# Kernel tuning notes

Measured on AMD Instinct MI355X. Metric: run time of the kernel, lower is better.

Reference implementation:

```python
import jax, jax.numpy as jnp
import numpy as np

B, CDD, L, T, H, NH = 16, 10, 64, 128, 768, 12
DH = H // NH          # head dim = 64
S = CDD * L + T       # full sequence = 768 (640 candidate tokens + 128 terms)


def setup_inputs() -> dict:
    key = jax.random.key(0)
    ks = jax.random.split(key, 7)
    w = 0.02
    return {
        "hidden_states": jax.random.normal(ks[0], (B, S, H), jnp.float32),
        "Wq": jax.random.normal(ks[1], (H, H), jnp.float32) * w,
        "bq": jax.random.normal(ks[2], (H,), jnp.float32) * w,
        "Wk": jax.random.normal(ks[3], (H, H), jnp.float32) * w,
        "bk": jax.random.normal(ks[4], (H,), jnp.float32) * w,
        "Wv": jax.random.normal(ks[5], (H, H), jnp.float32) * w,
        "bv": jax.random.normal(ks[6], (H,), jnp.float32) * w,
    }


def _one_pass_mask(dtype):
    # block-diagonal over candidates + dense global columns for terms
    block = jnp.kron(jnp.eye(CDD, dtype=dtype), jnp.ones((L, L), dtype=dtype))  # [CDD*L, CDD*L]
    return jnp.concatenate([block, jnp.ones((CDD * L, T), dtype=dtype)], axis=-1)  # [CDD*L, S]


def reference(hidden_states, Wq, bq, Wk, bk, Wv, bv):
    def split_heads(x):  # [B, s, H] -> [B, NH, s, DH]
        return x.reshape(B, -1, NH, DH).transpose(0, 2, 1, 3)

    attn_field = hidden_states[:, :-T]                     # [B, CDD*L, H] queries only
    q = split_heads(attn_field @ Wq.T + bq)                # [B, NH, CDD*L, DH]
    k = split_heads(hidden_states @ Wk.T + bk)             # [B, NH, S, DH]
    v = split_heads(hidden_states @ Wv.T + bv)             # [B, NH, S, DH]

    mask = _one_pass_mask(q.dtype)                         # [CDD*L, S]
    scale = 1.0 / np.sqrt(DH).astype(np.float32)
    # NOTE: original multiplies scores by the mask (masked entries become 0, not -inf)
    scores = jnp.einsum('bhqd,bhkd->bhqk', q, k) * scale * mask
    probs = jax.nn.softmax(scores, axis=-1)                # [B, NH, CDD*L, S]

    ctx = jnp.einsum('bhqk,bhkd->bhqd', probs, v)          # [B, NH, CDD*L, DH]
    ctx = jnp.concatenate([ctx, v[:, :, -T:]], axis=2)     # append term values untouched
    return ctx.transpose(0, 2, 1, 3).reshape(B, S, H)
```

## Files before the change

kernel.cpp:

```cpp
#include <hip/hip_runtime.h>

constexpr int Bb  = 16;
constexpr int CDD = 10;
constexpr int Lc  = 64;
constexpr int T   = 128;
constexpr int H   = 768;
constexpr int NH  = 12;
constexpr int DH  = 64;
constexpr int S   = 768;
constexpr int SQ  = 640;
constexpr int MROWS = Bb * S;

typedef __attribute__((ext_vector_type(8))) short bf16x8;
typedef __attribute__((ext_vector_type(4))) short bf16x4;
typedef __attribute__((ext_vector_type(4))) float f32x4;

__device__ inline unsigned short f2bf(float f) {
  unsigned u = __float_as_uint(f);
  u += 0x7fff + ((u >> 16) & 1);
  return (unsigned short)(u >> 16);
}
__device__ inline float bf2f(unsigned short h) {
  return __uint_as_float(((unsigned)h) << 16);
}

__device__ inline void gld_lds16(const void* g, void* l) {
  __builtin_amdgcn_global_load_lds(
      (const __attribute__((address_space(1))) void*)g,
      (__attribute__((address_space(3))) void*)l, 16, 0, 0);
}

__device__ inline bf16x8 ld_b64x2(const unsigned short* p) {
  union { bf16x8 v; bf16x4 h[2]; } u;
  u.h[0] = *(const bf16x4*)p;
  u.h[1] = *(const bf16x4*)(p + 4);
  return u.v;
}

constexpr int NX4 = MROWS * H / 4;
constexpr int NW4 = H * H / 4;
__global__ void convert_all(const float* __restrict__ X,
                            const float* __restrict__ Wq,
                            const float* __restrict__ Wk,
                            const float* __restrict__ Wv,
                            unsigned short* __restrict__ Xb,
                            unsigned short* __restrict__ Wb) {
  int i = blockIdx.x * blockDim.x + threadIdx.x;
  const int stride = gridDim.x * blockDim.x;
  const int total = NX4 + 3 * NW4;
  for (; i < total; i += stride) {
    const float* src;
    unsigned short* dst;
    int off;
    if (i < NX4) {
      src = X; dst = Xb; off = i;
    } else {
      int k = i - NX4;
      int w = k / NW4;
      off = k - w * NW4;
      src = (w == 0) ? Wq : (w == 1) ? Wk : Wv;
      dst = Wb + (size_t)w * H * H;
    }
    float4 v = ((const float4*)src)[off];
    ushort4 o;
    o.x = f2bf(v.x); o.y = f2bf(v.y); o.z = f2bf(v.z); o.w = f2bf(v.w);
    ((ushort4*)dst)[off] = o;
  }
}

__launch_bounds__(256, 4)
__global__ void qkv_gemm(const unsigned short* __restrict__ Xb,
                         const unsigned short* __restrict__ Wb,
                         const float* __restrict__ bq, const float* __restrict__ bk,
                         const float* __restrict__ bv,
                         unsigned short* __restrict__ Qb, unsigned short* __restrict__ Kb,
                         unsigned short* __restrict__ Vb,
                         float* __restrict__ part,
                         float* __restrict__ out) {
  const int z = blockIdx.z;
  if (z == 0 && (blockIdx.x % 6) == 5) return;
  const unsigned short* W = Wb + (size_t)z * H * H;
  const float* bias = (z == 0) ? bq : (z == 1) ? bk : bv;
  unsigned short* Y = (z == 0) ? Qb : (z == 1) ? Kb : Vb;

  const int i0 = blockIdx.x * 128;
  const int j0 = blockIdx.y * 128;
  const int tid = threadIdx.x;
  const int wave = tid >> 6, lane = tid & 63;
  const int wr = wave >> 1, wc = wave & 1;
  const int col = lane & 15, quad = lane >> 4;

  __shared__ unsigned short As[128 * 32];
  __shared__ unsigned short Bs[128 * 32];

  f32x4 acc[4][4];
#pragma unroll
  for (int i = 0; i < 4; i++)
#pragma unroll
    for (int j = 0; j < 4; j++) acc[i][j] = (f32x4){0.f, 0.f, 0.f, 0.f};

  const int rowA0 = tid >> 2, csA0 = tid & 3;
  const int rowA1 = (tid + 256) >> 2, csA1 = tid & 3;
  const int gcA0 = csA0 ^ ((rowA0 >> 1) & 3);
  const int gcA1 = csA1 ^ ((rowA1 >> 1) & 3);

  for (int kt = 0; kt < 24; kt++) {
    const int k0 = kt * 32;
    gld_lds16(Xb + (size_t)(i0 + rowA0) * H + k0 + gcA0 * 8, &As[tid * 8]);
    gld_lds16(Xb + (size_t)(i0 + rowA1) * H + k0 + gcA1 * 8, &As[(tid + 256) * 8]);
    gld_lds16(W  + (size_t)(j0 + rowA0) * H + k0 + gcA0 * 8, &Bs[tid * 8]);
    gld_lds16(W  + (size_t)(j0 + rowA1) * H + k0 + gcA1 * 8, &Bs[(tid + 256) * 8]);
    __builtin_amdgcn_s_waitcnt(0);
    __syncthreads();

    bf16x8 a[4], b[4];
#pragma unroll
    for (int mt = 0; mt < 4; mt++) {
      int r = wr * 64 + mt * 16 + col;
      a[mt] = *(const bf16x8*)&As[r * 32 + ((quad ^ ((r >> 1) & 3)) * 8)];
    }
#pragma unroll
    for (int nt = 0; nt < 4; nt++) {
      int r = wc * 64 + nt * 16 + col;
      b[nt] = *(const bf16x8*)&Bs[r * 32 + ((quad ^ ((r >> 1) & 3)) * 8)];
    }
#pragma unroll
    for (int mt = 0; mt < 4; mt++)
#pragma unroll
      for (int nt = 0; nt < 4; nt++)
        acc[mt][nt] = __builtin_amdgcn_mfma_f32_16x16x32_bf16(a[mt], b[nt], acc[mt][nt], 0, 0, 0);
    __syncthreads();
  }

  float colsum[4] = {0.f, 0.f, 0.f, 0.f};
#pragma unroll
  for (int mt = 0; mt < 4; mt++) {
#pragma unroll
    for (int nt = 0; nt < 4; nt++) {
      const int j = j0 + wc * 64 + nt * 16 + col;
      const float bj = bias[j];
#pragma unroll
      for (int r = 0; r < 4; r++) {
        const int i = i0 + wr * 64 + mt * 16 + quad * 4 + r;
        const float v = acc[mt][nt][r] + bj;
        Y[(size_t)i * H + j] = f2bf(v);
        if (z == 2) {
          colsum[nt] += v;
          int s = i - (i / S) * S;
          if (s >= SQ) out[(size_t)i * H + j] = v;
        }
      }
    }
  }
  if (z == 2) {
    const int b = blockIdx.x / 6;
#pragma unroll
    for (int nt = 0; nt < 4; nt++) {
      float s = colsum[nt];
      s += __shfl_xor(s, 16, 64);
      s += __shfl_xor(s, 32, 64);
      if (quad == 0) {
        const int j = j0 + wc * 64 + nt * 16 + col;
        atomicAdd(&part[b * H + j], s);
      }
    }
  }
}

__launch_bounds__(256, 3)
__global__ void attn_kernel(const unsigned short* __restrict__ Qb,
                            const unsigned short* __restrict__ Kb,
                            const unsigned short* __restrict__ Vb,
                            const float* __restrict__ part,
                            float* __restrict__ out) {
  const int bid = blockIdx.x;
  const int c = bid % CDD;
  const int h = (bid / CDD) % NH;
  const int b = bid / (CDD * NH);
  const int tid = threadIdx.x;
  const int wave = tid >> 6, lane = tid & 63;
  const int col = lane & 15, quad = lane >> 4;

  __shared__ __align__(16) char smem[51200];
  unsigned short* Vt = (unsigned short*)smem;
  unsigned short* Ps = (unsigned short*)(smem + 25088);
  float* red = (float*)(smem + 50176);

#pragma unroll
  for (int j = 0; j < 6; j++) {
    int s = tid + 256 * j;
    int key = s >> 3;
    int f0 = (s & 7) * 8;
    int gkey = (key < 64) ? (c * 64 + key) : (576 + key);
    union { int4 i4; unsigned short u[8]; } uv;
    uv.i4 = *(const int4*)(Vb + (size_t)(b * S + gkey) * H + h * DH + f0);
#pragma unroll
    for (int i = 0; i < 8; i++) Vt[(f0 + i) * 196 + key] = uv.u[i];
  }

  f32x4 sc[12];
#pragma unroll
  for (int n = 0; n < 12; n++) sc[n] = (f32x4){0.f, 0.f, 0.f, 0.f};
  {
    const unsigned short* qrow =
        Qb + (size_t)(b * S + c * 64 + wave * 16 + col) * H + h * DH;
    bf16x8 a0 = *(const bf16x8*)(qrow + quad * 8);
    bf16x8 a1 = *(const bf16x8*)(qrow + 32 + quad * 8);
#pragma unroll
    for (int n = 0; n < 12; n++) {
      const int rk = n * 16 + col;
      const int gkey = (rk < 64) ? (c * 64 + rk) : (576 + rk);
      const unsigned short* krow = Kb + (size_t)(b * S + gkey) * H + h * DH;
      bf16x8 b0 = *(const bf16x8*)(krow + quad * 8);
      bf16x8 b1 = *(const bf16x8*)(krow + 32 + quad * 8);
      sc[n] = __builtin_amdgcn_mfma_f32_16x16x32_bf16(a0, b0, sc[n], 0, 0, 0);
      sc[n] = __builtin_amdgcn_mfma_f32_16x16x32_bf16(a1, b1, sc[n], 0, 0, 0);
    }
  }

  float em[4], zin[4];
  {
    const float scale = 0.125f;
#pragma unroll
    for (int r = 0; r < 4; r++) {
      float mx = sc[0][r];
#pragma unroll
      for (int n = 1; n < 12; n++) mx = fmaxf(mx, sc[n][r]);
#pragma unroll
      for (int msk = 1; msk <= 8; msk <<= 1) mx = fmaxf(mx, __shfl_xor(mx, msk, 64));
      const float mrow = fmaxf(mx * scale, 0.f);
      float rs = 0.f;
#pragma unroll
      for (int n = 0; n < 12; n++) {
        float p = __expf(sc[n][r] * scale - mrow);
        sc[n][r] = p;
        rs += p;
      }
#pragma unroll
      for (int msk = 1; msk <= 8; msk <<= 1) rs += __shfl_xor(rs, msk, 64);
      const float e = __expf(-mrow);
      em[r] = e;
      zin[r] = 1.f / (rs + 576.f * e);
    }
  }

  __syncthreads();

  {
    int d = tid & 63, p = tid >> 6;
    float sum = 0.f;
    for (int k = p * 48; k < p * 48 + 48; k++) sum += bf2f(Vt[d * 196 + k]);
    red[tid] = sum;
  }
#pragma unroll
  for (int n = 0; n < 12; n++)
#pragma unroll
    for (int r = 0; r < 4; r++)
      Ps[(wave * 16 + quad * 4 + r) * 196 + n * 16 + col] = f2bf(sc[n][r]);
  __syncthreads();

  f32x4 o[4];
#pragma unroll
  for (int n2 = 0; n2 < 4; n2++) o[n2] = (f32x4){0.f, 0.f, 0.f, 0.f};
#pragma unroll
  for (int ks = 0; ks < 6; ks++) {
    bf16x8 a = ld_b64x2(&Ps[(wave * 16 + col) * 196 + ks * 32 + quad * 8]);
#pragma unroll
    for (int n2 = 0; n2 < 4; n2++) {
      bf16x8 bvv = ld_b64x2(&Vt[(n2 * 16 + col) * 196 + ks * 32 + quad * 8]);
      o[n2] = __builtin_amdgcn_mfma_f32_16x16x32_bf16(a, bvv, o[n2], 0, 0, 0);
    }
  }

#pragma unroll
  for (int n2 = 0; n2 < 4; n2++) {
    const int d = n2 * 16 + col;
    const float vc = part[b * H + h * DH + d] -
                     (red[d] + red[64 + d] + red[128 + d] + red[192 + d]);
#pragma unroll
    for (int r = 0; r < 4; r++) {
      const int m = wave * 16 + quad * 4 + r;
      const float val = (o[n2][r] + em[r] * vc) * zin[r];
      out[(size_t)(b * S + c * 64 + m) * H + h * DH + d] = val;
    }
  }
}

extern "C" void kernel_launch(void* const* d_in, const int* in_sizes, int n_in,
                              void* d_out, int out_size, void* d_ws, size_t ws_size,
                              hipStream_t stream) {
  const float* X  = (const float*)d_in[0];
  const float* Wq = (const float*)d_in[1];
  const float* bq = (const float*)d_in[2];
  const float* Wk = (const float*)d_in[3];
  const float* bk = (const float*)d_in[4];
  const float* Wv = (const float*)d_in[5];
  const float* bv = (const float*)d_in[6];
  float* out = (float*)d_out;

  char* ws = (char*)d_ws;
  unsigned short* Xb   = (unsigned short*)ws;
  unsigned short* Wb   = (unsigned short*)(ws + 18874368);
  unsigned short* Qb   = (unsigned short*)(ws + 22413312);
  unsigned short* Kb   = (unsigned short*)(ws + 41287680);
  unsigned short* Vb   = (unsigned short*)(ws + 60162048);
  float*          part = (float*)(ws + 79036416);

  hipMemsetAsync(part, 0, Bb * H * sizeof(float), stream);
  convert_all<<<2048, 256, 0, stream>>>(X, Wq, Wk, Wv, Xb, Wb);
  qkv_gemm<<<dim3(96, 6, 3), 256, 0, stream>>>(Xb, Wb, bq, bk, bv, Qb, Kb, Vb, part, out);
  attn_kernel<<<1920, 256, 0, stream>>>(Qb, Kb, Vb, part, out);
}
```

Measured before the change: 189.7 us.

## Move V column-sum into a separate partial-sum kernel and fold mask offset into P

The per-batch V column sums are no longer built with atomics in the QKV GEMM epilogue. A new kernel writes eight row-slice partial sums per batch, and the attention kernel adds them up, which removes the memset and the atomics. The attention kernel drops its shared-memory reduction over local V rows and one barrier by writing P minus the masked-entry weight into the bf16 P tile, so the MFMA pass yields the correction directly. In exchange there is an extra kernel launch, and the early return that skipped Q projection for term rows is gone, adding unused GEMM work. Storing p minus e in bf16 may also shift rounding.

```diff
diff --git a/kernel.cpp b/kernel.cpp
--- a/kernel.cpp
+++ b/kernel.cpp
@@ -75,10 +75,8 @@
                          const float* __restrict__ bv,
                          unsigned short* __restrict__ Qb, unsigned short* __restrict__ Kb,
                          unsigned short* __restrict__ Vb,
-                         float* __restrict__ part,
                          float* __restrict__ out) {
   const int z = blockIdx.z;
-  if (z == 0 && (blockIdx.x % 6) == 5) return;
   const unsigned short* W = Wb + (size_t)z * H * H;
   const float* bias = (z == 0) ? bq : (z == 1) ? bk : bv;
   unsigned short* Y = (z == 0) ? Qb : (z == 1) ? Kb : Vb;
@@ -132,7 +130,6 @@
     __syncthreads();
   }
 
-  float colsum[4] = {0.f, 0.f, 0.f, 0.f};
 #pragma unroll
   for (int mt = 0; mt < 4; mt++) {
 #pragma unroll
@@ -145,26 +142,24 @@
         const float v = acc[mt][nt][r] + bj;
         Y[(size_t)i * H + j] = f2bf(v);
         if (z == 2) {
-          colsum[nt] += v;
           int s = i - (i / S) * S;
           if (s >= SQ) out[(size_t)i * H + j] = v;
         }
       }
     }
   }
-  if (z == 2) {
-    const int b = blockIdx.x / 6;
-#pragma unroll
-    for (int nt = 0; nt < 4; nt++) {
-      float s = colsum[nt];
-      s += __shfl_xor(s, 16, 64);
-      s += __shfl_xor(s, 32, 64);
-      if (quad == 0) {
-        const int j = j0 + wc * 64 + nt * 16 + col;
-        atomicAdd(&part[b * H + j], s);
-      }
-    }
-  }
+}
+
+__global__ void vtot_partial(const unsigned short* __restrict__ Vb,
+                             float* __restrict__ part) {
+  const int b = blockIdx.x;
+  const int j = blockIdx.y * 256 + threadIdx.x;
+  const int rs = blockIdx.z;
+  const unsigned short* p = Vb + (size_t)(b * S + rs * 96) * H + j;
+  float s = 0.f;
+#pragma unroll 8
+  for (int r = 0; r < 96; r++) s += bf2f(p[(size_t)r * H]);
+  part[(size_t)(b * 8 + rs) * H + j] = s;
 }
 
 __launch_bounds__(256, 3)
@@ -181,10 +176,9 @@
   const int wave = tid >> 6, lane = tid & 63;
   const int col = lane & 15, quad = lane >> 4;
 
-  __shared__ __align__(16) char smem[51200];
+  __shared__ __align__(16) char smem[50176];
   unsigned short* Vt = (unsigned short*)smem;
   unsigned short* Ps = (unsigned short*)(smem + 25088);
-  float* red = (float*)(smem + 50176);
 
 #pragma unroll
   for (int j = 0; j < 6; j++) {
@@ -244,19 +238,22 @@
     }
   }
 
-  __syncthreads();
-
-  {
-    int d = tid & 63, p = tid >> 6;
-    float sum = 0.f;
-    for (int k = p * 48; k < p * 48 + 48; k++) sum += bf2f(Vt[d * 196 + k]);
-    red[tid] = sum;
-  }
+  float vtd[4];
+#pragma unroll
+  for (int n2 = 0; n2 < 4; n2++) {
+    const int d = n2 * 16 + col;
+    float s = 0.f;
+#pragma unroll
+    for (int rs = 0; rs < 8; rs++) s += part[(size_t)(b * 8 + rs) * H + h * DH + d];
+    vtd[n2] = s;
+  }
+
 #pragma unroll
   for (int n = 0; n < 12; n++)
 #pragma unroll
     for (int r = 0; r < 4; r++)
-      Ps[(wave * 16 + quad * 4 + r) * 196 + n * 16 + col] = f2bf(sc[n][r]);
+      Ps[(wave * 16 + quad * 4 + r) * 196 + n * 16 + col] = f2bf(sc[n][r] - em[r]);
+
   __syncthreads();
 
   f32x4 o[4];
@@ -275,12 +272,10 @@
 #pragma unroll
   for (int n2 = 0; n2 < 4; n2++) {
     const int d = n2 * 16 + col;
-    const float vc = part[b * H + h * DH + d] -
-                     (red[d] + red[64 + d] + red[128 + d] + red[192 + d]);
 #pragma unroll
     for (int r = 0; r < 4; r++) {
       const int m = wave * 16 + quad * 4 + r;
-      const float val = (o[n2][r] + em[r] * vc) * zin[r];
+      const float val = (o[n2][r] + em[r] * vtd[n2]) * zin[r];
       out[(size_t)(b * S + c * 64 + m) * H + h * DH + d] = val;
     }
   }
@@ -306,8 +301,8 @@
   unsigned short* Vb   = (unsigned short*)(ws + 60162048);
   float*          part = (float*)(ws + 79036416);
 
-  hipMemsetAsync(part, 0, Bb * H * sizeof(float), stream);
   convert_all<<<2048, 256, 0, stream>>>(X, Wq, Wk, Wv, Xb, Wb);
-  qkv_gemm<<<dim3(96, 6, 3), 256, 0, stream>>>(Xb, Wb, bq, bk, bv, Qb, Kb, Vb, part, out);
+  qkv_gemm<<<dim3(96, 6, 3), 256, 0, stream>>>(Xb, Wb, bq, bk, bv, Qb, Kb, Vb, out);
+  vtot_partial<<<dim3(16, 3, 8), 256, 0, stream>>>(Vb, part);
   attn_kernel<<<1920, 256, 0, stream>>>(Qb, Kb, Vb, part, out);
 }
```

New measurement: 194.8 us. +2.7%, slower.
